# Kernel optimization log

Hardware: AMD Instinct MI355X
Metric: run time of the kernel (lower is better)

Reference implementation:

```python
import jax, jax.numpy as jnp
import numpy as np


def setup_inputs() -> dict:
    key = jax.random.key(0)
    k1, k2 = jax.random.split(key)
    B, T, D = 16, 512, 384
    MAX_LEN = 4096
    x = jax.random.normal(k1, (B, T, D), dtype=jnp.float32)
    durations = jax.random.randint(k2, (B, T), 0, 8, dtype=jnp.int64)
    return {"x": x, "durations": durations, "max_len": MAX_LEN}


def reference(x, durations, max_len):
    # x: (B, T, D), durations: (B, T) int
    B, T, D = x.shape
    cum = jnp.cumsum(durations, axis=1)          # (B, T) exclusive-of-nothing cumulative ends
    mel_len = cum[:, -1]                         # (B,) actual (uncapped) frame lengths
    frames = jnp.arange(max_len)                 # (F,)
    # phoneme index owning each output frame: searchsorted on cumulative ends
    idx = jax.vmap(lambda c: jnp.searchsorted(c, frames, side='right'))(cum)  # (B, F)
    idx = jnp.clip(idx, 0, T - 1)
    out = jnp.take_along_axis(x, idx[:, :, None], axis=1)  # (B, F, D)
    # zero-pad frames beyond each item's length (and beyond max_len truncation)
    valid = frames[None, :] < jnp.minimum(mel_len, max_len)[:, None]  # (B, F)
    out = out * valid[:, :, None].astype(out.dtype)
    return out, mel_len
```

## Files before the change

kernel.cpp:

```cpp
#include <hip/hip_runtime.h>


#define B_ 16
#define T_ 512
#define D_ 384
#define MAXLEN_ 4096
#define ROWV4_ (D_ / 4)
#define OUT_ELEMS_ (B_ * MAXLEN_ * D_)
#define BLOCKS_PER_BATCH_ ((MAXLEN_ * ROWV4_) / 256)

__global__ __launch_bounds__(T_) void lr_scan_kernel(const int* __restrict__ dur,
                                                     int* __restrict__ cum_ws,
                                                     float* __restrict__ mel_out) {
    const int b = blockIdx.x, t = threadIdx.x;
    const int lane = t & 63, w = t >> 6;
    int v = dur[b * T_ + t];
    #pragma unroll
    for (int off = 1; off < 64; off <<= 1) {
        int n = __shfl_up(v, off);
        if (lane >= off) v += n;
    }
    __shared__ int wsum[8];
    if (lane == 63) wsum[w] = v;
    __syncthreads();
    if (t < 8) {
        int u = wsum[t];
        #pragma unroll
        for (int off = 1; off < 8; off <<= 1) {
            int n = __shfl_up(u, off);
            if (t >= off) u += n;
        }
        wsum[t] = u;
    }
    __syncthreads();
    const int cum = v + (w > 0 ? wsum[w - 1] : 0);
    cum_ws[b * T_ + t] = cum;
    if (t == T_ - 1) mel_out[b] = (float)cum;
}

__global__ __launch_bounds__(256) void lr_gather_kernel(const float4* __restrict__ x,
                                                        const int* __restrict__ cum_ws,
                                                        const int* __restrict__ max_len_p,
                                                        float4* __restrict__ out) {
    __shared__ int s[T_];
    const int t = threadIdx.x;
    const int b = blockIdx.x / BLOCKS_PER_BATCH_;
    const int* cb = cum_ws + b * T_;
    s[t] = cb[t];
    s[t + 256] = cb[t + 256];
    __syncthreads();

    const int g = blockIdx.x * 256 + t;
    const int row = g / ROWV4_;
    const int col = g - row * ROWV4_;
    const int f = row & (MAXLEN_ - 1);
    const int mel = s[T_ - 1];
    const int max_len = max_len_p[0];

    float4 v = make_float4(0.f, 0.f, 0.f, 0.f);
    if (f < mel && f < max_len) {
        int idx = 0;
        #pragma unroll
        for (int step = 256; step > 0; step >>= 1)
            if (s[idx + step - 1] <= f) idx += step;
        if (idx > T_ - 1) idx = T_ - 1;
        v = x[(b * T_ + idx) * ROWV4_ + col];
    }
    out[g] = v;
}

extern "C" void kernel_launch(void* const* d_in, const int* in_sizes, int n_in,
                              void* d_out, int out_size, void* d_ws, size_t ws_size,
                              hipStream_t stream) {
    const float* x = (const float*)d_in[0];
    const int* dur = (const int*)d_in[1];
    const int* max_len_p = (const int*)d_in[2];

    float* out = (float*)d_out;
    float* mel_out = out + OUT_ELEMS_;
    int* cum_ws = (int*)d_ws;

    lr_scan_kernel<<<B_, T_, 0, stream>>>(dur, cum_ws, mel_out);

    const int total_v4 = OUT_ELEMS_ / 4;
    lr_gather_kernel<<<total_v4 / 256, 256, 0, stream>>>(
        (const float4*)x, cum_ws, max_len_p, (float4*)out);
}
```

Before: 120.9 us.

## Compute frame indices once per block and gather 64 frames per block

Restructures the gather so each 384-thread block handles 64 frames of one batch. The per-frame binary search runs once per frame into shared memory instead of once per float4 element. Each thread then loops over 16 frames, reading the cached index and copying a row chunk. Output goes through nontemporal stores to avoid polluting cache. This removes redundant searches and shrinks the grid, in exchange for an extra barrier and fewer, larger blocks.

```diff
diff --git a/kernel.cpp b/kernel.cpp
--- a/kernel.cpp
+++ b/kernel.cpp
@@ -7,7 +7,12 @@
 #define MAXLEN_ 4096
 #define ROWV4_ (D_ / 4)
 #define OUT_ELEMS_ (B_ * MAXLEN_ * D_)
-#define BLOCKS_PER_BATCH_ ((MAXLEN_ * ROWV4_) / 256)
+
+#define FPB_ 64
+#define GT_ 384
+#define BPB_ (MAXLEN_ / FPB_)
+
+typedef float vf4 __attribute__((ext_vector_type(4)));
 
 __global__ __launch_bounds__(T_) void lr_scan_kernel(const int* __restrict__ dur,
                                                      int* __restrict__ cum_ws,
@@ -38,35 +43,49 @@
     if (t == T_ - 1) mel_out[b] = (float)cum;
 }
 
-__global__ __launch_bounds__(256) void lr_gather_kernel(const float4* __restrict__ x,
+__global__ __launch_bounds__(GT_) void lr_gather_kernel(const vf4* __restrict__ x,
                                                         const int* __restrict__ cum_ws,
                                                         const int* __restrict__ max_len_p,
-                                                        float4* __restrict__ out) {
+                                                        vf4* __restrict__ out) {
     __shared__ int s[T_];
+    __shared__ int sidx[FPB_];
     const int t = threadIdx.x;
-    const int b = blockIdx.x / BLOCKS_PER_BATCH_;
-    const int* cb = cum_ws + b * T_;
-    s[t] = cb[t];
-    s[t + 256] = cb[t + 256];
+    const int b = blockIdx.x / BPB_;
+    const int f0 = (blockIdx.x - b * BPB_) * FPB_;
+
+    if (t < T_ / 4)
+        ((int4*)s)[t] = ((const int4*)(cum_ws + b * T_))[t];
     __syncthreads();
 
-    const int g = blockIdx.x * 256 + t;
-    const int row = g / ROWV4_;
-    const int col = g - row * ROWV4_;
-    const int f = row & (MAXLEN_ - 1);
-    const int mel = s[T_ - 1];
-    const int max_len = max_len_p[0];
+    if (t < FPB_) {
+        const int f = f0 + t;
+        const int lim = min(s[T_ - 1], max_len_p[0]);
+        int idx = -1;
+        if (f < lim) {
+            idx = 0;
+            #pragma unroll
+            for (int step = 256; step > 0; step >>= 1)
+                if (s[idx + step - 1] <= f) idx += step;
+            if (idx > T_ - 1) idx = T_ - 1;
+        }
+        sidx[t] = idx;
+    }
+    __syncthreads();
 
-    float4 v = make_float4(0.f, 0.f, 0.f, 0.f);
-    if (f < mel && f < max_len) {
-        int idx = 0;
-        #pragma unroll
-        for (int step = 256; step > 0; step >>= 1)
-            if (s[idx + step - 1] <= f) idx += step;
-        if (idx > T_ - 1) idx = T_ - 1;
-        v = x[(b * T_ + idx) * ROWV4_ + col];
+    const int fl = t / 96;
+    const int col = t - fl * 96;
+    const vf4* xb = x + (size_t)(b * T_) * ROWV4_;
+    vf4* ob = out + ((size_t)b * MAXLEN_ + f0) * ROWV4_;
+    const vf4 zero = (vf4)(0.f);
+
+    #pragma unroll
+    for (int k = 0; k < FPB_ / 4; ++k) {
+        const int f = fl + 4 * k;
+        const int idx = sidx[f];
+        vf4 v = zero;
+        if (idx >= 0) v = xb[idx * ROWV4_ + col];
+        __builtin_nontemporal_store(v, &ob[f * ROWV4_ + col]);
     }
-    out[g] = v;
 }
 
 extern "C" void kernel_launch(void* const* d_in, const int* in_sizes, int n_in,
@@ -82,7 +101,6 @@
 
     lr_scan_kernel<<<B_, T_, 0, stream>>>(dur, cum_ws, mel_out);
 
-    const int total_v4 = OUT_ELEMS_ / 4;
-    lr_gather_kernel<<<total_v4 / 256, 256, 0, stream>>>(
-        (const float4*)x, cum_ws, max_len_p, (float4*)out);
+    lr_gather_kernel<<<B_ * BPB_, GT_, 0, stream>>>(
+        (const vf4*)x, cum_ws, max_len_p, (vf4*)out);
 }
```

After: 129.6 us. +7.3%, slower.
